# Optimization experiments

Hardware: AMD Instinct MI355X
Metric: run time of the kernel (lower is better)

Reference implementation:

```python
import math
import jax, jax.numpy as jnp
import numpy as np

B, S, H, NH = 2, 2048, 1024, 16
HD = H // NH


def setup_inputs() -> dict:
    key = jax.random.key(0)
    k1, k2, k3 = jax.random.split(key, 3)
    scale = 1.0 / math.sqrt(H)
    return {
        "hidden_states": jax.random.normal(k1, (B, S, H), dtype=jnp.float32),
        "attention_mask": jnp.ones((B, 1, S, S), dtype=jnp.float32),
        "qkv_w": jax.random.normal(k2, (3 * H, H), dtype=jnp.float32) * scale,
        "qkv_b": jnp.zeros((3 * H,), dtype=jnp.float32),
        "dense_w": jax.random.normal(k3, (H, H), dtype=jnp.float32) * scale,
        "dense_b": jnp.zeros((H,), dtype=jnp.float32),
    }


def reference(hidden_states, attention_mask, qkv_w, qkv_b, dense_w, dense_b):
    # qkv projection: torch Linear y = x @ W^T + b
    mixed = hidden_states @ qkv_w.T + qkv_b            # [B,S,3H]
    mixed = mixed.reshape(B, S, NH, 3 * HD).transpose(0, 2, 1, 3)  # [B,NH,S,3HD]
    q, k, v = jnp.split(mixed, 3, axis=-1)             # each [B,NH,S,HD]
    scores = jnp.einsum("bhqd,bhkd->bhqk", q, k) / math.sqrt(HD)
    scores = scores * attention_mask - 10000.0 * (1.0 - attention_mask)
    probs = jax.nn.softmax(scores, axis=-1)            # dropout p=0 -> identity
    ctx = jnp.einsum("bhqk,bhkd->bhqd", probs, v)      # [B,NH,S,HD]
    ctx = ctx.transpose(0, 2, 1, 3).reshape(B, S, H)
    out = ctx @ dense_w.T + dense_b                    # output dropout p=0
    return out
```

## Files before the change

kernel.cpp:

```cpp
#include <hip/hip_runtime.h>
#include <hip/hip_bf16.h>
#include <stdint.h>

#define BB 2
#define SS 2048
#define HH 1024
#define NHH 16
#define HDD 64
#define MM (BB*SS)
#define N1 (3*HH)
#define NT (SS/64)
#define LOG2E 1.44269504f

using bf16 = __hip_bfloat16;
typedef __attribute__((ext_vector_type(8))) short bf16x8;
typedef __attribute__((ext_vector_type(4))) float f32x4;

__device__ inline unsigned short f2bfu(float f) {
  union { bf16 h; unsigned short u; } c;
  c.h = __float2bfloat16(f);
  return c.u;
}

__device__ inline unsigned int cvtpk(float lo, float hi) {
  unsigned int r;
  asm("v_cvt_pk_bf16_f32 %0, %1, %2" : "=v"(r) : "v"(lo), "v"(hi));
  return r;
}

__device__ inline void load_lds16(const void* g, void* l) {
  __builtin_amdgcn_global_load_lds(
      (const __attribute__((address_space(1))) void*)g,
      (__attribute__((address_space(3))) void*)l, 16, 0, 0);
}

__device__ inline f32x4 mfma16(bf16x8 a, bf16x8 b, f32x4 c) {
  return __builtin_amdgcn_mfma_f32_16x16x32_bf16(a, b, c, 0, 0, 0);
}

__global__ __launch_bounds__(256) void cvt3_f32_bf16(const float* __restrict__ a,
                                                     unsigned short* __restrict__ ao, int na4,
                                                     const float* __restrict__ bsrc,
                                                     unsigned short* __restrict__ bo, int nb4,
                                                     const float* __restrict__ c,
                                                     unsigned short* __restrict__ co, int nc4) {
  int total = na4 + nb4 + nc4;
  int st = gridDim.x * blockDim.x;
  for (int i = blockIdx.x * blockDim.x + threadIdx.x; i < total; i += st) {
    const float* in; unsigned short* out; int j = i;
    if (j < na4) { in = a; out = ao; }
    else if (j < na4 + nb4) { j -= na4; in = bsrc; out = bo; }
    else { j -= na4 + nb4; in = c; out = co; }
    float4 v = reinterpret_cast<const float4*>(in)[j];
    ushort4 o;
    o.x = f2bfu(v.x); o.y = f2bfu(v.y); o.z = f2bfu(v.z); o.w = f2bfu(v.w);
    reinterpret_cast<ushort4*>(out)[j] = o;
  }
}

__global__ __launch_bounds__(256) void mask_flags_kernel(const float* __restrict__ mask,
                                                         unsigned char* __restrict__ flags) {
  int t = blockIdx.x;
  int b = t >> 10, qt = (t >> 5) & 31, kt = t & 31;
  const float* mb = mask + ((size_t)b * SS + qt * 64) * SS + kt * 64;
  int row = threadIdx.x >> 2, c0 = (threadIdx.x & 3) * 16;
  int ok = 1;
#pragma unroll
  for (int j = 0; j < 4; ++j) {
    float4 v = *reinterpret_cast<const float4*>(mb + (size_t)row * SS + c0 + j * 4);
    ok &= (v.x == 1.f) & (v.y == 1.f) & (v.z == 1.f) & (v.w == 1.f);
  }
  ok = __all(ok);
  __shared__ int s[4];
  if ((threadIdx.x & 63) == 0) s[threadIdx.x >> 6] = ok;
  __syncthreads();
  if (threadIdx.x == 0) flags[t] = (unsigned char)(s[0] & s[1] & s[2] & s[3]);
}

__global__ __launch_bounds__(256) void vtrans_kernel(const unsigned short* __restrict__ mixed,
                                                     unsigned short* __restrict__ vT) {
  __shared__ unsigned short t[64 * 72];
  const int st = blockIdx.x, bh = blockIdx.y;
  const int b = bh >> 4, h = bh & 15;
  const int r = threadIdx.x >> 2, c0 = (threadIdx.x & 3) * 16;

  const unsigned short* src = mixed + ((size_t)(b * SS) + st * 64) * N1 + h * 192 + 128;
  union { bf16x8 v; unsigned short u[8]; } A, B;
  A.v = *reinterpret_cast<const bf16x8*>(src + (size_t)r * N1 + c0);
  B.v = *reinterpret_cast<const bf16x8*>(src + (size_t)r * N1 + c0 + 8);
#pragma unroll
  for (int j = 0; j < 8; ++j) t[(c0 + j) * 72 + r] = A.u[j];
#pragma unroll
  for (int j = 0; j < 8; ++j) t[(c0 + 8 + j) * 72 + r] = B.u[j];
  __syncthreads();

  unsigned short* dst = vT + ((size_t)bh * HDD + r) * SS + st * 64 + c0;
  bf16x8 o0 = *reinterpret_cast<const bf16x8*>(&t[r * 72 + c0]);
  bf16x8 o1 = *reinterpret_cast<const bf16x8*>(&t[r * 72 + c0 + 8]);
  *reinterpret_cast<bf16x8*>(dst) = o0;
  *reinterpret_cast<bf16x8*>(dst + 8) = o1;
}

template <bool OUT_BF16>
__global__ __launch_bounds__(256) void gemm_bt(const unsigned short* __restrict__ A,
                                               const unsigned short* __restrict__ Bt,
                                               const float* __restrict__ bias,
                                               void* __restrict__ Cv,
                                               int Ndim, int Kdim) {
  __shared__ __align__(16) unsigned short As[128 * 64];
  __shared__ __align__(16) unsigned short Bs[128 * 64];

  const int tid = threadIdx.x;
  const int wave = tid >> 6, lane = tid & 63;
  const int m0 = blockIdx.x * 128;
  const int n0 = blockIdx.y * 128;
  const int wm = (wave >> 1) * 64, wn = (wave & 1) * 64;
  const int lrow = lane & 15;
  const int g = lane >> 4;
  const int r4 = (lane >> 4) * 4;
  const int x0 = (g ^ (lrow & 7)) << 3;
  const int x1 = ((g + 4) ^ (lrow & 7)) << 3;

  f32x4 acc[4][4];
  const f32x4 z = {0.f, 0.f, 0.f, 0.f};
  for (int i = 0; i < 4; ++i)
    for (int j = 0; j < 4; ++j) acc[i][j] = z;

  for (int k0 = 0; k0 < Kdim; k0 += 64) {
#pragma unroll
    for (int it = 0; it < 4; ++it) {
      int idx = it * 256 + tid;
      int row = idx >> 3, seg = idx & 7;
      int sw = (seg ^ (row & 7)) << 3;
      load_lds16(A + (size_t)(m0 + row) * Kdim + k0 + sw, &As[row * 64 + seg * 8]);
      load_lds16(Bt + (size_t)(n0 + row) * Kdim + k0 + sw, &Bs[row * 64 + seg * 8]);
    }
    __syncthreads();

    bf16x8 af[4], bfr[4];
#pragma unroll
    for (int i = 0; i < 4; ++i)
      af[i] = *reinterpret_cast<const bf16x8*>(&As[(wm + i * 16 + lrow) * 64 + x0]);
#pragma unroll
    for (int j = 0; j < 4; ++j)
      bfr[j] = *reinterpret_cast<const bf16x8*>(&Bs[(wn + j * 16 + lrow) * 64 + x0]);
#pragma unroll
    for (int i = 0; i < 4; ++i)
#pragma unroll
      for (int j = 0; j < 4; ++j)
        acc[i][j] = mfma16(af[i], bfr[j], acc[i][j]);
#pragma unroll
    for (int i = 0; i < 4; ++i)
      af[i] = *reinterpret_cast<const bf16x8*>(&As[(wm + i * 16 + lrow) * 64 + x1]);
#pragma unroll
    for (int j = 0; j < 4; ++j)
      bfr[j] = *reinterpret_cast<const bf16x8*>(&Bs[(wn + j * 16 + lrow) * 64 + x1]);
#pragma unroll
    for (int i = 0; i < 4; ++i)
#pragma unroll
      for (int j = 0; j < 4; ++j)
        acc[i][j] = mfma16(af[i], bfr[j], acc[i][j]);
    __syncthreads();
  }

#pragma unroll
  for (int i = 0; i < 4; ++i) {
#pragma unroll
    for (int j = 0; j < 4; ++j) {
      int col = n0 + wn + j * 16 + lrow;
      float bv = bias[col];
#pragma unroll
      for (int r = 0; r < 4; ++r) {
        int row = m0 + wm + i * 16 + r4 + r;
        float v = acc[i][j][r] + bv;
        if (OUT_BF16) {
          ((unsigned short*)Cv)[(size_t)row * Ndim + col] = f2bfu(v);
        } else {
          ((float*)Cv)[(size_t)row * Ndim + col] = v;
        }
      }
    }
  }
}

__global__ __launch_bounds__(256, 4) void attn_kernel(const unsigned short* __restrict__ mixed,
                                                      const unsigned short* __restrict__ vT,
                                                      const float* __restrict__ mask,
                                                      const unsigned char* __restrict__ flags,
                                                      unsigned short* __restrict__ ctx) {
  __shared__ __align__(16) unsigned short Ks[2][64 * 64];
  __shared__ __align__(16) unsigned short Vt[2][64 * 64];
  __shared__ __align__(16) unsigned short QP[64 * 64];

  const int tid = threadIdx.x, wave = tid >> 6, lane = tid & 63;
  const int ql = lane & 15;
  const int g = lane >> 4;
  const int q0 = blockIdx.x * 64;
  const int bh = blockIdx.y;
  const int b = bh / NHH, hh = bh % NHH;

  const unsigned short* qbase = mixed + (size_t)(b * SS) * N1 + hh * 192;
  const unsigned short* kbase = qbase + 64;
  const unsigned short* vtbase = vT + ((size_t)(b * NHH + hh) * HDD) * SS;
  const float* mbase = mask + (size_t)b * SS * SS;
  const unsigned char* fl = flags + ((size_t)b * 32 + blockIdx.x) * 32;

  const int srow = tid >> 3, sseg = tid & 7;
  const int swst = (sseg ^ (srow & 7)) << 3;

  load_lds16(qbase + (size_t)(q0 + srow) * N1 + swst, &QP[srow * 64 + sseg * 8]);
  load_lds16(qbase + (size_t)(q0 + 32 + srow) * N1 + swst, &QP[(32 + srow) * 64 + sseg * 8]);
  load_lds16(kbase + (size_t)srow * N1 + swst, &Ks[0][srow * 64 + sseg * 8]);
  load_lds16(kbase + (size_t)(32 + srow) * N1 + swst, &Ks[0][(32 + srow) * 64 + sseg * 8]);
  load_lds16(vtbase + (size_t)srow * SS + swst, &Vt[0][srow * 64 + sseg * 8]);
  load_lds16(vtbase + (size_t)(32 + srow) * SS + swst, &Vt[0][(32 + srow) * 64 + sseg * 8]);
  __syncthreads();

  const int qrow = wave * 16 + ql;
  const bf16x8 qf0 = *reinterpret_cast<const bf16x8*>(
      &QP[qrow * 64 + ((g ^ (qrow & 7)) << 3)]);
  const bf16x8 qf1 = *reinterpret_cast<const bf16x8*>(
      &QP[qrow * 64 + (((g + 4) ^ (qrow & 7)) << 3)]);
  __syncthreads();

  const int s0 = (g ^ (ql & 7)) << 3;
  const int s1 = ((g + 4) ^ (ql & 7)) << 3;
  const unsigned short* KrA = &Ks[0][ql * 64 + s0];
  const unsigned short* KrB = &Ks[0][ql * 64 + s1];
  const unsigned short* VrA = &Vt[0][ql * 64 + s0];
  const unsigned short* VrB = &Vt[0][ql * 64 + s1];
  unsigned short* Ps = &QP[wave * 1024];
  const int X = (ql & 7) << 3;
  unsigned short* Pw0 = &Ps[ql * 64 + ((4 * g) ^ X)];
  unsigned short* Pw1 = &Ps[ql * 64 + ((16 + 4 * g) ^ X)];
  unsigned short* Pw2 = &Ps[ql * 64 + ((32 + 4 * g) ^ X)];
  unsigned short* Pw3 = &Ps[ql * 64 + ((48 + 4 * g) ^ X)];
  const unsigned short* Pr0 = &Ps[ql * 64 + ((8 * g) ^ X)];
  const unsigned short* Pr1 = &Ps[ql * 64 + ((32 + 8 * g) ^ X)];

  const unsigned short* kpre = kbase + (size_t)(64 + srow) * N1 + swst;
  const unsigned short* vpre = vtbase + (size_t)srow * SS + 64 + swst;

  f32x4 oacc[4];
  const f32x4 z = {0.f, 0.f, 0.f, 0.f};
  for (int fd = 0; fd < 4; ++fd) oacc[fd] = z;
  float lsum = 0.f;
  const float C2 = 0.125f * LOG2E;

#define TILE_BODY(CUR_, KT_, HAVENEXT_)                                         \
  {                                                                             \
    const int kt_ = (KT_);                                                      \
    if (HAVENEXT_) {                                                            \
      load_lds16(kpre, &Ks[(CUR_)^1][srow * 64 + sseg * 8]);                    \
      load_lds16(kpre + 32 * N1, &Ks[(CUR_)^1][(32 + srow) * 64 + sseg * 8]);   \
      load_lds16(vpre, &Vt[(CUR_)^1][srow * 64 + sseg * 8]);                    \
      load_lds16(vpre + 32 * SS, &Vt[(CUR_)^1][(32 + srow) * 64 + sseg * 8]);   \
    }                                                                           \
    kpre += 64 * N1; vpre += 64;                                                \
    f32x4 sacc[4];                                                              \
    __builtin_amdgcn_s_setprio(1);                                              \
    _Pragma("unroll")                                                           \
    for (int n = 0; n < 4; ++n) {                                               \
      bf16x8 k0 = *reinterpret_cast<const bf16x8*>(KrA + (CUR_)*4096 + n*1024); \
      bf16x8 k1 = *reinterpret_cast<const bf16x8*>(KrB + (CUR_)*4096 + n*1024); \
      sacc[n] = mfma16(k0, qf0, z);                                             \
      sacc[n] = mfma16(k1, qf1, sacc[n]);                                       \
    }                                                                           \
    __builtin_amdgcn_s_setprio(0);                                              \
    const bool allones = fl[kt_] != 0;                                          \
    float pv[4][4];                                                             \
    if (allones) {                                                              \
      _Pragma("unroll")                                                         \
      for (int n = 0; n < 4; ++n)                                               \
        _Pragma("unroll")                                                       \
        for (int r = 0; r < 4; ++r)                                             \
          pv[n][r] = exp2f(sacc[n][r] * C2);                                    \
    } else {                                                                    \
      int qq = q0 + wave * 16 + ql;                                             \
      _Pragma("unroll")                                                         \
      for (int n = 0; n < 4; ++n)                                               \
        _Pragma("unroll")                                                       \
        for (int r = 0; r < 4; ++r) {                                           \
          int kk = kt_ * 64 + 16 * n + 4 * g + r;                               \
          float mv = mbase[(size_t)qq * SS + kk];                               \
          float s = sacc[n][r] * 0.125f;                                        \
          pv[n][r] = exp2f((s * mv - 10000.f * (1.f - mv)) * LOG2E);            \
        }                                                                       \
    }                                                                           \
    {                                                                           \
      float t00 = (pv[0][0] + pv[0][1]) + (pv[0][2] + pv[0][3]);                \
      float t01 = (pv[1][0] + pv[1][1]) + (pv[1][2] + pv[1][3]);                \
      float t10 = (pv[2][0] + pv[2][1]) + (pv[2][2] + pv[2][3]);                \
      float t11 = (pv[3][0] + pv[3][1]) + (pv[3][2] + pv[3][3]);                \
      lsum += (t00 + t01) + (t10 + t11);                                        \
    }                                                                           \
    { uint2 w; w.x = cvtpk(pv[0][0], pv[0][1]); w.y = cvtpk(pv[0][2], pv[0][3]);\
      *reinterpret_cast<uint2*>(Pw0) = w; }                                     \
    { uint2 w; w.x = cvtpk(pv[1][0], pv[1][1]); w.y = cvtpk(pv[1][2], pv[1][3]);\
      *reinterpret_cast<uint2*>(Pw1) = w; }                                     \
    { uint2 w; w.x = cvtpk(pv[2][0], pv[2][1]); w.y = cvtpk(pv[2][2], pv[2][3]);\
      *reinterpret_cast<uint2*>(Pw2) = w; }                                     \
    { uint2 w; w.x = cvtpk(pv[3][0], pv[3][1]); w.y = cvtpk(pv[3][2], pv[3][3]);\
      *reinterpret_cast<uint2*>(Pw3) = w; }                                     \
    bf16x8 pa0 = *reinterpret_cast<const bf16x8*>(Pr0);                         \
    bf16x8 pa1 = *reinterpret_cast<const bf16x8*>(Pr1);                         \
    __builtin_amdgcn_s_setprio(1);                                              \
    _Pragma("unroll")                                                           \
    for (int fd = 0; fd < 4; ++fd) {                                            \
      bf16x8 bv0 = *reinterpret_cast<const bf16x8*>(VrA + (CUR_)*4096 + fd*1024);\
      bf16x8 bv1 = *reinterpret_cast<const bf16x8*>(VrB + (CUR_)*4096 + fd*1024);\
      oacc[fd] = mfma16(pa0, bv0, oacc[fd]);                                    \
      oacc[fd] = mfma16(pa1, bv1, oacc[fd]);                                    \
    }                                                                           \
    __builtin_amdgcn_s_setprio(0);                                              \
    __syncthreads();                                                            \
  }

  for (int kt = 0; kt < NT; kt += 2) {
    TILE_BODY(0, kt, true)
    TILE_BODY(1, kt + 1, (kt + 2 < NT))
  }
#undef TILE_BODY

  float lrun = lsum;
  lrun += __shfl_xor(lrun, 16, 64);
  lrun += __shfl_xor(lrun, 32, 64);
  float invl = 1.f / lrun;
#pragma unroll
  for (int r = 0; r < 4; ++r) {
    float inv = __shfl(invl, g * 4 + r, 64);
    int qq = q0 + wave * 16 + g * 4 + r;
    unsigned short* cp = ctx + (size_t)(b * SS + qq) * HH + hh * HDD;
#pragma unroll
    for (int fd = 0; fd < 4; ++fd)
      cp[fd * 16 + ql] = f2bfu(oacc[fd][r] * inv);
  }
}

extern "C" void kernel_launch(void* const* d_in, const int* in_sizes, int n_in,
                              void* d_out, int out_size, void* d_ws, size_t ws_size,
                              hipStream_t stream) {
  const float* hs      = (const float*)d_in[0];
  const float* mask    = (const float*)d_in[1];
  const float* qkv_w   = (const float*)d_in[2];
  const float* qkv_b   = (const float*)d_in[3];
  const float* dense_w = (const float*)d_in[4];
  const float* dense_b = (const float*)d_in[5];
  float* out = (float*)d_out;

  char* ws = (char*)d_ws;
  unsigned short* hs_b     = (unsigned short*)(ws);
  unsigned short* qkvw_b   = (unsigned short*)(ws + 8388608);
  unsigned short* densew_b = (unsigned short*)(ws + 14680064);
  unsigned short* mixed_b  = (unsigned short*)(ws + 16777216);
  unsigned short* ctx_b    = (unsigned short*)(ws + 41943040);
  unsigned char*  flags    = (unsigned char*)(ws + 50331648);
  unsigned short* vT_b     = (unsigned short*)(ws + 50335744);

  cvt3_f32_bf16<<<2048, 256, 0, stream>>>(hs, hs_b, (MM * HH) / 4,
                                          qkv_w, qkvw_b, (N1 * HH) / 4,
                                          dense_w, densew_b, (HH * HH) / 4);
  mask_flags_kernel<<<BB * 32 * 32, 256, 0, stream>>>(mask, flags);

  gemm_bt<true><<<dim3(MM / 128, N1 / 128), 256, 0, stream>>>(
      hs_b, qkvw_b, qkv_b, mixed_b, N1, HH);

  vtrans_kernel<<<dim3(SS / 64, BB * NHH), 256, 0, stream>>>(mixed_b, vT_b);

  attn_kernel<<<dim3(SS / 64, BB * NHH), 256, 0, stream>>>(
      mixed_b, vT_b, mask, flags, ctx_b);

  gemm_bt<false><<<dim3(MM / 128, HH / 128), 256, 0, stream>>>(
      ctx_b, densew_b, dense_b, out, HH, HH);
}
```

Baseline: 149.2 us.

## Rework attention kernel with 32x32 MFMA, 128-query blocks and split-K across waves

The attention kernel moves from 16x16x32 to 32x32x16 bf16 MFMA tiles and grows blocks to 512 threads covering 128 queries. Each group of waves handles one half of the key range, and the two partial outputs and softmax sums are combined through LDS at the end. Probabilities are passed to the PV MFMA through register lane shuffles instead of an LDS round-trip. This aims to cut LDS traffic and per-instruction overhead and to get more MFMA throughput, at the cost of higher register pressure, a final reduction step, and fewer blocks in the grid.

```diff
diff --git a/kernel.cpp b/kernel.cpp
--- a/kernel.cpp
+++ b/kernel.cpp
@@ -9,12 +9,12 @@
 #define HDD 64
 #define MM (BB*SS)
 #define N1 (3*HH)
-#define NT (SS/64)
 #define LOG2E 1.44269504f
 
 using bf16 = __hip_bfloat16;
 typedef __attribute__((ext_vector_type(8))) short bf16x8;
 typedef __attribute__((ext_vector_type(4))) float f32x4;
+typedef __attribute__((ext_vector_type(16))) float f32x16;
 
 __device__ inline unsigned short f2bfu(float f) {
   union { bf16 h; unsigned short u; } c;
@@ -36,6 +36,9 @@
 
 __device__ inline f32x4 mfma16(bf16x8 a, bf16x8 b, f32x4 c) {
   return __builtin_amdgcn_mfma_f32_16x16x32_bf16(a, b, c, 0, 0, 0);
+}
+__device__ inline f32x16 mfma32(bf16x8 a, bf16x8 b, f32x16 c) {
+  return __builtin_amdgcn_mfma_f32_32x32x16_bf16(a, b, c, 0, 0, 0);
 }
 
 __global__ __launch_bounds__(256) void cvt3_f32_bf16(const float* __restrict__ a,
@@ -183,19 +186,18 @@
   }
 }
 
-__global__ __launch_bounds__(256, 4) void attn_kernel(const unsigned short* __restrict__ mixed,
-                                                      const unsigned short* __restrict__ vT,
-                                                      const float* __restrict__ mask,
-                                                      const unsigned char* __restrict__ flags,
-                                                      unsigned short* __restrict__ ctx) {
-  __shared__ __align__(16) unsigned short Ks[2][64 * 64];
-  __shared__ __align__(16) unsigned short Vt[2][64 * 64];
-  __shared__ __align__(16) unsigned short QP[64 * 64];
+__global__ void attn_kernel(const unsigned short* __restrict__ mixed,
+                            const unsigned short* __restrict__ vT,
+                            const float* __restrict__ mask,
+                            const unsigned char* __restrict__ flags,
+                            unsigned short* __restrict__ ctx) {
+  __shared__ __align__(16) unsigned short Ks[2][2][64 * 64];
+  __shared__ __align__(16) unsigned short Vs[2][2][64 * 64];
 
   const int tid = threadIdx.x, wave = tid >> 6, lane = tid & 63;
-  const int ql = lane & 15;
-  const int g = lane >> 4;
-  const int q0 = blockIdx.x * 64;
+  const int qg = wave & 3, kh = wave >> 2;
+  const int l31 = lane & 31, h = lane >> 5;
+  const int q0 = blockIdx.x * 128;
   const int bh = blockIdx.y;
   const int b = bh / NHH, hh = bh % NHH;
 
@@ -203,137 +205,196 @@
   const unsigned short* kbase = qbase + 64;
   const unsigned short* vtbase = vT + ((size_t)(b * NHH + hh) * HDD) * SS;
   const float* mbase = mask + (size_t)b * SS * SS;
-  const unsigned char* fl = flags + ((size_t)b * 32 + blockIdx.x) * 32;
-
-  const int srow = tid >> 3, sseg = tid & 7;
-  const int swst = (sseg ^ (srow & 7)) << 3;
-
-  load_lds16(qbase + (size_t)(q0 + srow) * N1 + swst, &QP[srow * 64 + sseg * 8]);
-  load_lds16(qbase + (size_t)(q0 + 32 + srow) * N1 + swst, &QP[(32 + srow) * 64 + sseg * 8]);
-  load_lds16(kbase + (size_t)srow * N1 + swst, &Ks[0][srow * 64 + sseg * 8]);
-  load_lds16(kbase + (size_t)(32 + srow) * N1 + swst, &Ks[0][(32 + srow) * 64 + sseg * 8]);
-  load_lds16(vtbase + (size_t)srow * SS + swst, &Vt[0][srow * 64 + sseg * 8]);
-  load_lds16(vtbase + (size_t)(32 + srow) * SS + swst, &Vt[0][(32 + srow) * 64 + sseg * 8]);
-  __syncthreads();
-
-  const int qrow = wave * 16 + ql;
-  const bf16x8 qf0 = *reinterpret_cast<const bf16x8*>(
-      &QP[qrow * 64 + ((g ^ (qrow & 7)) << 3)]);
-  const bf16x8 qf1 = *reinterpret_cast<const bf16x8*>(
-      &QP[qrow * 64 + (((g + 4) ^ (qrow & 7)) << 3)]);
-  __syncthreads();
-
-  const int s0 = (g ^ (ql & 7)) << 3;
-  const int s1 = ((g + 4) ^ (ql & 7)) << 3;
-  const unsigned short* KrA = &Ks[0][ql * 64 + s0];
-  const unsigned short* KrB = &Ks[0][ql * 64 + s1];
-  const unsigned short* VrA = &Vt[0][ql * 64 + s0];
-  const unsigned short* VrB = &Vt[0][ql * 64 + s1];
-  unsigned short* Ps = &QP[wave * 1024];
-  const int X = (ql & 7) << 3;
-  unsigned short* Pw0 = &Ps[ql * 64 + ((4 * g) ^ X)];
-  unsigned short* Pw1 = &Ps[ql * 64 + ((16 + 4 * g) ^ X)];
-  unsigned short* Pw2 = &Ps[ql * 64 + ((32 + 4 * g) ^ X)];
-  unsigned short* Pw3 = &Ps[ql * 64 + ((48 + 4 * g) ^ X)];
-  const unsigned short* Pr0 = &Ps[ql * 64 + ((8 * g) ^ X)];
-  const unsigned short* Pr1 = &Ps[ql * 64 + ((32 + 8 * g) ^ X)];
-
-  const unsigned short* kpre = kbase + (size_t)(64 + srow) * N1 + swst;
-  const unsigned short* vpre = vtbase + (size_t)srow * SS + 64 + swst;
-
-  f32x4 oacc[4];
-  const f32x4 z = {0.f, 0.f, 0.f, 0.f};
-  for (int fd = 0; fd < 4; ++fd) oacc[fd] = z;
+  const unsigned char* fl = flags + ((size_t)b * 32 + blockIdx.x * 2 + (qg >> 1)) * 32 + kh * 16;
+
+  const int srow = (tid >> 3) & 63, sseg = tid & 7;
+  const int sw = (sseg ^ (srow & 7)) << 3;
+
+  {
+    unsigned short* Qtmp = &Ks[0][0][0];
+    load_lds16(qbase + (size_t)(q0 + srow) * N1 + sw, &Qtmp[srow * 64 + sseg * 8]);
+    load_lds16(qbase + (size_t)(q0 + 64 + srow) * N1 + sw, &Qtmp[(64 + srow) * 64 + sseg * 8]);
+  }
+  __syncthreads();
+  const int qrow = qg * 32 + l31;
+  const int xq = l31 & 7;
+  const int o0 = ((2 * 0 + h) ^ xq) << 3;
+  const int o1 = ((2 * 1 + h) ^ xq) << 3;
+  const int o2 = ((2 * 2 + h) ^ xq) << 3;
+  const int o3 = ((2 * 3 + h) ^ xq) << 3;
+  bf16x8 qf0, qf1, qf2, qf3;
+  {
+    const unsigned short* Qtmp = &Ks[0][0][0];
+    qf0 = *reinterpret_cast<const bf16x8*>(&Qtmp[qrow * 64 + o0]);
+    qf1 = *reinterpret_cast<const bf16x8*>(&Qtmp[qrow * 64 + o1]);
+    qf2 = *reinterpret_cast<const bf16x8*>(&Qtmp[qrow * 64 + o2]);
+    qf3 = *reinterpret_cast<const bf16x8*>(&Qtmp[qrow * 64 + o3]);
+  }
+  __syncthreads();
+
+  load_lds16(kbase + (size_t)srow * N1 + sw,          &Ks[0][0][srow * 64 + sseg * 8]);
+  load_lds16(kbase + (size_t)(1024 + srow) * N1 + sw, &Ks[1][0][srow * 64 + sseg * 8]);
+  load_lds16(vtbase + (size_t)srow * SS + sw,         &Vs[0][0][srow * 64 + sseg * 8]);
+  load_lds16(vtbase + (size_t)srow * SS + 1024 + sw,  &Vs[1][0][srow * 64 + sseg * 8]);
+  __syncthreads();
+
+  const unsigned short* KrA = &Ks[kh][0][l31 * 64];
+  const unsigned short* KrB = &Ks[kh][0][(32 + l31) * 64];
+  const unsigned short* Vr0 = &Vs[kh][0][l31 * 64];
+  const unsigned short* Vr1 = &Vs[kh][0][(32 + l31) * 64];
+
+  const unsigned short* kp0 = kbase + (size_t)(64 + srow) * N1 + sw;
+  const unsigned short* kp1 = kbase + (size_t)(1088 + srow) * N1 + sw;
+  const unsigned short* vp0 = vtbase + (size_t)srow * SS + 64 + sw;
+  const unsigned short* vp1 = vtbase + (size_t)srow * SS + 1088 + sw;
+
+  f32x16 oacc0, oacc1;
+#pragma unroll
+  for (int i = 0; i < 16; ++i) { oacc0[i] = 0.f; oacc1[i] = 0.f; }
   float lsum = 0.f;
   const float C2 = 0.125f * LOG2E;
 
-#define TILE_BODY(CUR_, KT_, HAVENEXT_)                                         \
+#define TILE(CUR_, I_, HAVENEXT_)                                               \
   {                                                                             \
-    const int kt_ = (KT_);                                                      \
+    const int i_ = (I_);                                                        \
     if (HAVENEXT_) {                                                            \
-      load_lds16(kpre, &Ks[(CUR_)^1][srow * 64 + sseg * 8]);                    \
-      load_lds16(kpre + 32 * N1, &Ks[(CUR_)^1][(32 + srow) * 64 + sseg * 8]);   \
-      load_lds16(vpre, &Vt[(CUR_)^1][srow * 64 + sseg * 8]);                    \
-      load_lds16(vpre + 32 * SS, &Vt[(CUR_)^1][(32 + srow) * 64 + sseg * 8]);   \
-    }                                                                           \
-    kpre += 64 * N1; vpre += 64;                                                \
-    f32x4 sacc[4];                                                              \
-    __builtin_amdgcn_s_setprio(1);                                              \
-    _Pragma("unroll")                                                           \
-    for (int n = 0; n < 4; ++n) {                                               \
-      bf16x8 k0 = *reinterpret_cast<const bf16x8*>(KrA + (CUR_)*4096 + n*1024); \
-      bf16x8 k1 = *reinterpret_cast<const bf16x8*>(KrB + (CUR_)*4096 + n*1024); \
-      sacc[n] = mfma16(k0, qf0, z);                                             \
-      sacc[n] = mfma16(k1, qf1, sacc[n]);                                       \
-    }                                                                           \
-    __builtin_amdgcn_s_setprio(0);                                              \
-    const bool allones = fl[kt_] != 0;                                          \
-    float pv[4][4];                                                             \
+      load_lds16(kp0, &Ks[0][(CUR_)^1][srow * 64 + sseg * 8]);                  \
+      load_lds16(kp1, &Ks[1][(CUR_)^1][srow * 64 + sseg * 8]);                  \
+      load_lds16(vp0, &Vs[0][(CUR_)^1][srow * 64 + sseg * 8]);                  \
+      load_lds16(vp1, &Vs[1][(CUR_)^1][srow * 64 + sseg * 8]);                  \
+    }                                                                           \
+    kp0 += 64 * N1; kp1 += 64 * N1; vp0 += 64; vp1 += 64;                       \
+    f32x16 sa0, sa1;                                                            \
+    {                                                                           \
+      bf16x8 kA0 = *reinterpret_cast<const bf16x8*>(KrA + (CUR_)*4096 + o0);    \
+      bf16x8 kB0 = *reinterpret_cast<const bf16x8*>(KrB + (CUR_)*4096 + o0);    \
+      bf16x8 kA1 = *reinterpret_cast<const bf16x8*>(KrA + (CUR_)*4096 + o1);    \
+      bf16x8 kB1 = *reinterpret_cast<const bf16x8*>(KrB + (CUR_)*4096 + o1);    \
+      bf16x8 kA2 = *reinterpret_cast<const bf16x8*>(KrA + (CUR_)*4096 + o2);    \
+      bf16x8 kB2 = *reinterpret_cast<const bf16x8*>(KrB + (CUR_)*4096 + o2);    \
+      bf16x8 kA3 = *reinterpret_cast<const bf16x8*>(KrA + (CUR_)*4096 + o3);    \
+      bf16x8 kB3 = *reinterpret_cast<const bf16x8*>(KrB + (CUR_)*4096 + o3);    \
+      __builtin_amdgcn_s_setprio(1);                                           \
+      f32x16 zz;                                                                \
+      _Pragma("unroll")                                                         \
+      for (int i = 0; i < 16; ++i) zz[i] = 0.f;                                 \
+      sa0 = mfma32(kA0, qf0, zz);  sa1 = mfma32(kB0, qf0, zz);                  \
+      sa0 = mfma32(kA1, qf1, sa0); sa1 = mfma32(kB1, qf1, sa1);                 \
+      sa0 = mfma32(kA2, qf2, sa0); sa1 = mfma32(kB2, qf2, sa1);                 \
+      sa0 = mfma32(kA3, qf3, sa0); sa1 = mfma32(kB3, qf3, sa1);                 \
+      __builtin_amdgcn_s_setprio(0);                                           \
+    }                                                                           \
+    const bool allones = fl[i_] != 0;                                           \
+    float pv0[16], pv1[16];                                                     \
     if (allones) {                                                              \
       _Pragma("unroll")                                                         \
-      for (int n = 0; n < 4; ++n)                                               \
-        _Pragma("unroll")                                                       \
-        for (int r = 0; r < 4; ++r)                                             \
-          pv[n][r] = exp2f(sacc[n][r] * C2);                                    \
+      for (int r = 0; r < 16; ++r) {                                            \
+        pv0[r] = exp2f(sa0[r] * C2);                                            \
+        pv1[r] = exp2f(sa1[r] * C2);                                            \
+      }                                                                         \
     } else {                                                                    \
-      int qq = q0 + wave * 16 + ql;                                             \
+      int qq = q0 + qg * 32 + l31;                                              \
+      int kt64 = (kh * 16 + i_) * 64;                                           \
       _Pragma("unroll")                                                         \
-      for (int n = 0; n < 4; ++n)                                               \
-        _Pragma("unroll")                                                       \
-        for (int r = 0; r < 4; ++r) {                                           \
-          int kk = kt_ * 64 + 16 * n + 4 * g + r;                               \
-          float mv = mbase[(size_t)qq * SS + kk];                               \
-          float s = sacc[n][r] * 0.125f;                                        \
-          pv[n][r] = exp2f((s * mv - 10000.f * (1.f - mv)) * LOG2E);            \
-        }                                                                       \
+      for (int r = 0; r < 16; ++r) {                                            \
+        int krow = (r & 3) + 8 * (r >> 2) + 4 * h;                              \
+        float mv0 = mbase[(size_t)qq * SS + kt64 + krow];                       \
+        float mv1 = mbase[(size_t)qq * SS + kt64 + 32 + krow];                  \
+        float s0 = sa0[r] * 0.125f, s1 = sa1[r] * 0.125f;                       \
+        pv0[r] = exp2f((s0 * mv0 - 10000.f * (1.f - mv0)) * LOG2E);             \
+        pv1[r] = exp2f((s1 * mv1 - 10000.f * (1.f - mv1)) * LOG2E);             \
+      }                                                                         \
     }                                                                           \
     {                                                                           \
-      float t00 = (pv[0][0] + pv[0][1]) + (pv[0][2] + pv[0][3]);                \
-      float t01 = (pv[1][0] + pv[1][1]) + (pv[1][2] + pv[1][3]);                \
-      float t10 = (pv[2][0] + pv[2][1]) + (pv[2][2] + pv[2][3]);                \
-      float t11 = (pv[3][0] + pv[3][1]) + (pv[3][2] + pv[3][3]);                \
-      lsum += (t00 + t01) + (t10 + t11);                                        \
-    }                                                                           \
-    { uint2 w; w.x = cvtpk(pv[0][0], pv[0][1]); w.y = cvtpk(pv[0][2], pv[0][3]);\
-      *reinterpret_cast<uint2*>(Pw0) = w; }                                     \
-    { uint2 w; w.x = cvtpk(pv[1][0], pv[1][1]); w.y = cvtpk(pv[1][2], pv[1][3]);\
-      *reinterpret_cast<uint2*>(Pw1) = w; }                                     \
-    { uint2 w; w.x = cvtpk(pv[2][0], pv[2][1]); w.y = cvtpk(pv[2][2], pv[2][3]);\
-      *reinterpret_cast<uint2*>(Pw2) = w; }                                     \
-    { uint2 w; w.x = cvtpk(pv[3][0], pv[3][1]); w.y = cvtpk(pv[3][2], pv[3][3]);\
-      *reinterpret_cast<uint2*>(Pw3) = w; }                                     \
-    bf16x8 pa0 = *reinterpret_cast<const bf16x8*>(Pr0);                         \
-    bf16x8 pa1 = *reinterpret_cast<const bf16x8*>(Pr1);                         \
-    __builtin_amdgcn_s_setprio(1);                                              \
+      float t0 = 0.f, t1 = 0.f;                                                 \
+      _Pragma("unroll")                                                         \
+      for (int r = 0; r < 16; r += 4)                                           \
+        t0 += (pv0[r] + pv0[r+1]) + (pv0[r+2] + pv0[r+3]);                      \
+      _Pragma("unroll")                                                         \
+      for (int r = 0; r < 16; r += 4)                                           \
+        t1 += (pv1[r] + pv1[r+1]) + (pv1[r+2] + pv1[r+3]);                      \
+      lsum += t0 + t1;                                                          \
+    }                                                                           \
+                 \
+    unsigned int Lo[2][4], Hi[2][4];                                            \
     _Pragma("unroll")                                                           \
-    for (int fd = 0; fd < 4; ++fd) {                                            \
-      bf16x8 bv0 = *reinterpret_cast<const bf16x8*>(VrA + (CUR_)*4096 + fd*1024);\
-      bf16x8 bv1 = *reinterpret_cast<const bf16x8*>(VrB + (CUR_)*4096 + fd*1024);\
-      oacc[fd] = mfma16(pa0, bv0, oacc[fd]);                                    \
-      oacc[fd] = mfma16(pa1, bv1, oacc[fd]);                                    \
-    }                                                                           \
-    __builtin_amdgcn_s_setprio(0);                                              \
+    for (int m = 0; m < 4; ++m) {                                               \
+      Lo[0][m] = cvtpk(pv0[4*m+0], pv0[4*m+1]);                                 \
+      Hi[0][m] = cvtpk(pv0[4*m+2], pv0[4*m+3]);                                 \
+      Lo[1][m] = cvtpk(pv1[4*m+0], pv1[4*m+1]);                                 \
+      Hi[1][m] = cvtpk(pv1[4*m+2], pv1[4*m+3]);                                 \
+    }                                                                           \
+    bf16x8 pa[4];                                                               \
+    _Pragma("unroll")                                                           \
+    for (int ks = 0; ks < 4; ++ks) {                                            \
+      int kb = ks >> 1, s = ks & 1;                                             \
+      unsigned int sendL = h ? Lo[kb][2*s] : Lo[kb][2*s+1];                     \
+      unsigned int recvL = __shfl_xor(sendL, 32, 64);                           \
+      unsigned int w0 = h ? recvL : Lo[kb][2*s];                                \
+      unsigned int w2 = h ? Lo[kb][2*s+1] : recvL;                              \
+      unsigned int sendH = h ? Hi[kb][2*s] : Hi[kb][2*s+1];                     \
+      unsigned int recvH = __shfl_xor(sendH, 32, 64);                           \
+      unsigned int w1 = h ? recvH : Hi[kb][2*s];                                \
+      unsigned int w3 = h ? Hi[kb][2*s+1] : recvH;                              \
+      union { bf16x8 v; unsigned int w[4]; } U;                                 \
+      U.w[0] = w0; U.w[1] = w1; U.w[2] = w2; U.w[3] = w3;                       \
+      pa[ks] = U.v;                                                             \
+    }                                                                           \
+                                                  \
+    {                                                                           \
+      bf16x8 bv00 = *reinterpret_cast<const bf16x8*>(Vr0 + (CUR_)*4096 + o0);   \
+      bf16x8 bv10 = *reinterpret_cast<const bf16x8*>(Vr1 + (CUR_)*4096 + o0);   \
+      bf16x8 bv01 = *reinterpret_cast<const bf16x8*>(Vr0 + (CUR_)*4096 + o1);   \
+      bf16x8 bv11 = *reinterpret_cast<const bf16x8*>(Vr1 + (CUR_)*4096 + o1);   \
+      bf16x8 bv02 = *reinterpret_cast<const bf16x8*>(Vr0 + (CUR_)*4096 + o2);   \
+      bf16x8 bv12 = *reinterpret_cast<const bf16x8*>(Vr1 + (CUR_)*4096 + o2);   \
+      bf16x8 bv03 = *reinterpret_cast<const bf16x8*>(Vr0 + (CUR_)*4096 + o3);   \
+      bf16x8 bv13 = *reinterpret_cast<const bf16x8*>(Vr1 + (CUR_)*4096 + o3);   \
+      __builtin_amdgcn_s_setprio(1);                                           \
+      oacc0 = mfma32(pa[0], bv00, oacc0); oacc1 = mfma32(pa[0], bv10, oacc1);   \
+      oacc0 = mfma32(pa[1], bv01, oacc0); oacc1 = mfma32(pa[1], bv11, oacc1);   \
+      oacc0 = mfma32(pa[2], bv02, oacc0); oacc1 = mfma32(pa[2], bv12, oacc1);   \
+      oacc0 = mfma32(pa[3], bv03, oacc0); oacc1 = mfma32(pa[3], bv13, oacc1);   \
+      __builtin_amdgcn_s_setprio(0);                                           \
+    }                                                                           \
     __syncthreads();                                                            \
   }
 
-  for (int kt = 0; kt < NT; kt += 2) {
-    TILE_BODY(0, kt, true)
-    TILE_BODY(1, kt + 1, (kt + 2 < NT))
-  }
-#undef TILE_BODY
-
-  float lrun = lsum;
-  lrun += __shfl_xor(lrun, 16, 64);
-  lrun += __shfl_xor(lrun, 32, 64);
-  float invl = 1.f / lrun;
-#pragma unroll
-  for (int r = 0; r < 4; ++r) {
-    float inv = __shfl(invl, g * 4 + r, 64);
-    int qq = q0 + wave * 16 + g * 4 + r;
-    unsigned short* cp = ctx + (size_t)(b * SS + qq) * HH + hh * HDD;
-#pragma unroll
-    for (int fd = 0; fd < 4; ++fd)
-      cp[fd * 16 + ql] = f2bfu(oacc[fd][r] * inv);
+  for (int it = 0; it < 16; it += 2) {
+    TILE(0, it, true)
+    TILE(1, it + 1, (it + 2 < 16))
+  }
+#undef TILE
+
+  float* Ms = reinterpret_cast<float*>(&Ks[0][0][0]);
+  float* Ls = reinterpret_cast<float*>(&Vs[0][0][0]);
+  if (kh == 1) {
+#pragma unroll
+    for (int i = 0; i < 16; ++i) {
+      Ms[(qg * 32 + i) * 64 + lane] = oacc0[i];
+      Ms[(qg * 32 + 16 + i) * 64 + lane] = oacc1[i];
+    }
+    Ls[qg * 64 + lane] = lsum;
+  }
+  __syncthreads();
+  if (kh == 0) {
+#pragma unroll
+    for (int i = 0; i < 16; ++i) {
+      oacc0[i] += Ms[(qg * 32 + i) * 64 + lane];
+      oacc1[i] += Ms[(qg * 32 + 16 + i) * 64 + lane];
+    }
+    lsum += Ls[qg * 64 + lane];
+    lsum += __shfl_xor(lsum, 32, 64);
+    float invl = 1.f / lsum;
+#pragma unroll
+    for (int r = 0; r < 16; ++r) {
+      int qr = (r & 3) + 8 * (r >> 2) + 4 * h;
+      float inv = __shfl(invl, qr, 64);
+      int qq = q0 + qg * 32 + qr;
+      unsigned short* cp = ctx + (size_t)(b * SS + qq) * HH + hh * HDD;
+      cp[l31] = f2bfu(oacc0[r] * inv);
+      cp[32 + l31] = f2bfu(oacc1[r] * inv);
+    }
   }
 }
 
@@ -367,7 +428,7 @@
 
   vtrans_kernel<<<dim3(SS / 64, BB * NHH), 256, 0, stream>>>(mixed_b, vT_b);
 
-  attn_kernel<<<dim3(SS / 64, BB * NHH), 256, 0, stream>>>(
+  attn_kernel<<<dim3(SS / 128, BB * NHH), 512, 0, stream>>>(
       mixed_b, vT_b, mask, flags, ctx_b);
 
   gemm_bt<false><<<dim3(MM / 128, HH / 128), 256, 0, stream>>>(
```

Result: slower. 263.6 us, median of 2 (+76.6%).
